# Performance work log

Measured on AMD Instinct MI355X. Metric: run time of the kernel, lower is better.

## Reference

```python
import jax, jax.numpy as jnp
import numpy as np

VOCAB, D_MODEL, N_STATE, H_HEADS, LAYERS = 64, 512, 32, 16, 4
EXPAND = 2
D_INNER = EXPAND * D_MODEL          # 1024
P_HEAD = D_INNER // H_HEADS         # 64
CONV_DIM = D_INNER + 2 * N_STATE    # x, B, C share the depthwise conv
K_CONV = 4
D_IN_PROJ = 2 * D_INNER + 2 * N_STATE + H_HEADS  # z, x, B, C, dt
BATCH, SEQ = 4, 1024
EPS = 1e-5


def rmsnorm(x, w):
    return x * jax.lax.rsqrt(jnp.mean(x * x, axis=-1, keepdims=True) + EPS) * w


def silu(x):
    return x * jax.nn.sigmoid(x)


def causal_depthwise_conv(x, w, b):
    # x: [B,L,C], w: [C,K], b: [C]; causal (left) padding, depthwise groups
    xt = jnp.transpose(x, (0, 2, 1))  # [B,C,L]
    out = jax.lax.conv_general_dilated(xt, w[:, None, :], (1,), [(K_CONV - 1, 0)], feature_group_count=w.shape[0])
    return jnp.transpose(out, (0, 2, 1)) + b


def ssd(xh, dt, A, Bm, Cm, Dp):
    # Mamba2 SSD recurrence. xh [B,L,H,P], dt [B,L,H], A [H], Bm/Cm [B,L,N], Dp [H]
    dA = jnp.exp(dt * A)              # decay per (batch, step, head)
    dtx = dt[..., None] * xh          # [B,L,H,P]

    def step(h, inp):
        dA_t, dtx_t, B_t, C_t = inp
        # h: [B,H,P,N]
        h = dA_t[:, :, None, None] * h + dtx_t[..., None] * B_t[:, None, None, :]
        y = jnp.einsum('bhpn,bn->bhp', h, C_t)
        return h, y

    h0 = jnp.zeros((xh.shape[0], H_HEADS, P_HEAD, N_STATE), xh.dtype)
    _, ys = jax.lax.scan(step, h0, (jnp.moveaxis(dA, 1, 0), jnp.moveaxis(dtx, 1, 0), jnp.moveaxis(Bm, 1, 0), jnp.moveaxis(Cm, 1, 0)))
    return jnp.moveaxis(ys, 0, 1) + xh * Dp[None, None, :, None]


def mamba_block(x, norm_w, W_in, b_in, conv_w, conv_b, dt_bias, A_log, Dp, gnorm_w, W_out, b_out):
    res = x
    u = rmsnorm(x, norm_w)
    zxbcdt = u @ W_in + b_in                                # [B,L,D_IN_PROJ]
    z = zxbcdt[..., :D_INNER]
    xBC = zxbcdt[..., D_INNER:D_INNER + CONV_DIM]
    dt = zxbcdt[..., D_INNER + CONV_DIM:]                   # [B,L,H]
    xBC = silu(causal_depthwise_conv(xBC, conv_w, conv_b))
    xc = xBC[..., :D_INNER]
    Bm = xBC[..., D_INNER:D_INNER + N_STATE]
    Cm = xBC[..., D_INNER + N_STATE:]
    dt = jax.nn.softplus(dt + dt_bias)
    xh = xc.reshape(xc.shape[0], xc.shape[1], H_HEADS, P_HEAD)
    y = ssd(xh, dt, -jnp.exp(A_log), Bm, Cm, Dp)
    y = y.reshape(y.shape[0], y.shape[1], D_INNER)
    y = rmsnorm(y * silu(z), gnorm_w)                       # gated RMSNorm
    return res + y @ W_out + b_out


def forward(input_tokens, emb, norm_w, W_in, b_in, conv_w, conv_b, dt_bias, A_log, D_param, gnorm_w, W_out, b_out, head_w, head_b):
    h = emb[input_tokens]
    for i in range(LAYERS):
        h = mamba_block(h, norm_w[i], W_in[i], b_in[i], conv_w[i], conv_b[i], dt_bias[i], A_log[i], D_param[i], gnorm_w[i], W_out[i], b_out[i])
    return h @ head_w + head_b


def setup_inputs() -> dict:
    key = jax.random.key(0)
    ks = jax.random.split(key, 8)
    s = 0.02
    return {
        'input_tokens': jax.random.randint(ks[0], (BATCH, SEQ), 0, VOCAB),
        'emb': jax.random.normal(ks[1], (VOCAB, D_MODEL), jnp.float32) * s,
        'norm_w': jnp.ones((LAYERS, D_MODEL), jnp.float32),
        'W_in': jax.random.normal(ks[2], (LAYERS, D_MODEL, D_IN_PROJ), jnp.float32) * s,
        'b_in': jnp.zeros((LAYERS, D_IN_PROJ), jnp.float32),
        'conv_w': jax.random.normal(ks[3], (LAYERS, CONV_DIM, K_CONV), jnp.float32) * 0.1,
        'conv_b': jnp.zeros((LAYERS, CONV_DIM), jnp.float32),
        'dt_bias': jnp.tile(jnp.log(jnp.expm1(jnp.linspace(0.001, 0.1, H_HEADS, dtype=jnp.float32))), (LAYERS, 1)),
        'A_log': jnp.tile(jnp.log(jnp.arange(1, H_HEADS + 1, dtype=jnp.float32)), (LAYERS, 1)),
        'D_param': jnp.ones((LAYERS, H_HEADS), jnp.float32),
        'gnorm_w': jnp.ones((LAYERS, D_INNER), jnp.float32),
        'W_out': jax.random.normal(ks[4], (LAYERS, D_INNER, D_MODEL), jnp.float32) * s,
        'b_out': jnp.zeros((LAYERS, D_MODEL), jnp.float32),
        'head_w': jax.random.normal(ks[5], (D_MODEL, VOCAB), jnp.float32) * s,
        'head_b': jnp.zeros((VOCAB,), jnp.float32),
    }


def reference(input_tokens, emb, norm_w, W_in, b_in, conv_w, conv_b, dt_bias, A_log, D_param, gnorm_w, W_out, b_out, head_w, head_b):
    return forward(input_tokens, emb, norm_w, W_in, b_in, conv_w, conv_b, dt_bias, A_log, D_param, gnorm_w, W_out, b_out, head_w, head_b)
```

## Files before the change

kernel.cpp:

```cpp
#include <hip/hip_runtime.h>
#include <hip/hip_bf16.h>

#define VOCAB     64
#define D_MODEL   512
#define N_STATE   32
#define H_HEADS   16
#define LAYERS    4
#define D_INNER   1024
#define P_HEAD    64
#define CONV_DIM  1088
#define K_CONV    4
#define D_IN_PROJ 2128
#define NPAD_IN   2176
#define NPAD_HEAD 64
#define BATCH     4
#define SEQ       1024
#define NTOK      (BATCH*SEQ)
#define EPS       1e-5f
#define CL        64
#define NC        (SEQ/CL)
#define PSTR      80

typedef __bf16 bf16x8 __attribute__((ext_vector_type(8)));
typedef float  f32x4  __attribute__((ext_vector_type(4)));

__device__ __forceinline__ float sigmoidf_(float x) { return 1.f / (1.f + __expf(-x)); }
__device__ __forceinline__ float softplusf_(float x) { return (x > 20.f) ? x : log1pf(__expf(x)); }

__device__ __forceinline__ void gload_lds16(const void* g, void* l) {
  __builtin_amdgcn_global_load_lds((const __attribute__((address_space(1))) void*)g,
                                   (__attribute__((address_space(3))) void*)l,
                                   16, 0, 0);
}

__device__ __forceinline__ int xcd_lin() {
  return (blockIdx.x & 7) * ((int)gridDim.x >> 3) + ((int)blockIdx.x >> 3);
}

__global__ __launch_bounds__(256) void prep_kernel(
    const float* __restrict__ W_in, const float* __restrict__ W_out,
    const float* __restrict__ head_w,
    const float* __restrict__ norm_w, const float* __restrict__ gnorm_w,
    __bf16* __restrict__ WtIn, __bf16* __restrict__ WtOut, __bf16* __restrict__ WtHead,
    const int* __restrict__ tok, const float* __restrict__ emb,
    float* __restrict__ h, __bf16* __restrict__ hbf) {
  int b = blockIdx.x;
  if (b >= 6432) {
    int eb = b - 6432;
    int wv = threadIdx.x >> 6, lane = threadIdx.x & 63;
    int tokid = eb * 4 + wv;
    const float* er = emb + (size_t)tok[tokid] * D_MODEL;
    f32x4 v0 = *(const f32x4*)(er + lane * 8);
    f32x4 v1 = *(const f32x4*)(er + lane * 8 + 4);
    float* hr = h + (size_t)tokid * D_MODEL;
    *(f32x4*)(hr + lane * 8) = v0;
    *(f32x4*)(hr + lane * 8 + 4) = v1;
    bf16x8 o8;
    #pragma unroll
    for (int k = 0; k < 4; k++) { o8[k] = (__bf16)v0[k]; o8[4 + k] = (__bf16)v1[k]; }
    *(bf16x8*)(hbf + (size_t)tokid * D_MODEL + lane * 8) = o8;
    return;
  }
  const float* W; const float* fold; __bf16* Wt; int K, N, Npad, bx, by;
  if (b < 4352) {
    int z = b / 1088, r = b % 1088;
    bx = r % 68; by = r / 68;
    W = W_in + (size_t)z * D_MODEL * D_IN_PROJ;
    fold = norm_w + (size_t)z * D_MODEL;
    Wt = WtIn + (size_t)z * NPAD_IN * D_MODEL;
    K = D_MODEL; N = D_IN_PROJ; Npad = NPAD_IN;
  } else if (b < 6400) {
    int r = b - 4352; int z = r / 512; r %= 512;
    bx = r % 16; by = r / 16;
    W = W_out + (size_t)z * D_INNER * D_MODEL;
    fold = gnorm_w + (size_t)z * D_INNER;
    Wt = WtOut + (size_t)z * D_MODEL * D_INNER;
    K = D_INNER; N = D_MODEL; Npad = D_MODEL;
  } else {
    int r = b - 6400;
    bx = r % 2; by = r / 2;
    W = head_w; fold = nullptr; Wt = WtHead;
    K = D_MODEL; N = VOCAB; Npad = NPAD_HEAD;
  }
  __shared__ float T[32][33];
  int n0 = bx * 32, k0 = by * 32;
  int tx = threadIdx.x & 31, ty = threadIdx.x >> 5;
  #pragma unroll
  for (int i = 0; i < 4; i++) {
    int n = n0 + tx;
    T[ty + i * 8][tx] = (n < N) ? W[(size_t)(k0 + ty + i * 8) * N + n] : 0.f;
  }
  __syncthreads();
  float fs = fold ? fold[k0 + tx] : 1.f;
  #pragma unroll
  for (int i = 0; i < 4; i++)
    Wt[(size_t)(n0 + ty + i * 8) * K + k0 + tx] = (__bf16)(T[tx][ty + i * 8] * fs);
}

#define TK 64
__global__ __launch_bounds__(256) void gemm64_kernel(
    const __bf16* __restrict__ A, const __bf16* __restrict__ Bt,
    const float* __restrict__ bias, const float* __restrict__ res,
    float* __restrict__ C, __bf16* __restrict__ Cbf,
    float inv_norm_dim, int nbx, int K, int N, int ldc) {
  __shared__ __bf16 As[2][64 * TK];
  __shared__ __bf16 Bs[2][64 * TK];
  int tid = threadIdx.x;
  int lane = tid & 63, wave = tid >> 6;
  int wm = wave >> 1, wn = wave & 1;
  int q = lane >> 4, l16 = lane & 15;
  int lin = xcd_lin();
  int bx = lin % nbx, by = lin / nbx;
  size_t row0 = (size_t)by * 64;
  int col0 = bx * 64;
  const __bf16* Ab = A + row0 * K;
  const __bf16* Bb = Bt + (size_t)col0 * K;

  auto stage = [&](int buf, int kk) {
    #pragma unroll
    for (int r = 0; r < 2; r++) {
      int lin2 = r * 256 + tid;
      size_t goff = (size_t)(lin2 >> 3) * K + kk + (lin2 & 7) * 8;
      gload_lds16(Ab + goff, &As[buf][lin2 * 8]);
      gload_lds16(Bb + goff, &Bs[buf][lin2 * 8]);
    }
  };

  f32x4 acc[2][2];
  #pragma unroll
  for (int i = 0; i < 2; i++)
    #pragma unroll
    for (int j = 0; j < 2; j++) acc[i][j] = (f32x4){0.f, 0.f, 0.f, 0.f};
  float ssqa[2] = {0.f, 0.f};

  stage(0, 0);
  int cur = 0;
  for (int k0 = 0; k0 < K; k0 += TK) {
    if (k0 + TK < K) {
      stage(cur ^ 1, k0 + TK);
      asm volatile("s_waitcnt vmcnt(4)" ::: "memory");
    } else {
      asm volatile("s_waitcnt vmcnt(0)" ::: "memory");
    }
    __builtin_amdgcn_s_barrier();
    #pragma unroll
    for (int ks = 0; ks < 2; ks++) {
      bf16x8 af[2], bfv[2];
      #pragma unroll
      for (int i = 0; i < 2; i++) {
        af[i] = *(const bf16x8*)(&As[cur][(wm * 32 + i * 16 + l16) * TK + ks * 32 + q * 8]);
        #pragma unroll
        for (int k = 0; k < 8; k++) { float v = (float)af[i][k]; ssqa[i] += v * v; }
      }
      #pragma unroll
      for (int j = 0; j < 2; j++)
        bfv[j] = *(const bf16x8*)(&Bs[cur][(wn * 32 + j * 16 + l16) * TK + ks * 32 + q * 8]);
      #pragma unroll
      for (int i = 0; i < 2; i++)
        #pragma unroll
        for (int j = 0; j < 2; j++)
          acc[i][j] = __builtin_amdgcn_mfma_f32_16x16x32_bf16(af[i], bfv[j], acc[i][j], 0, 0, 0);
    }
    __builtin_amdgcn_s_barrier();
    cur ^= 1;
  }

  #pragma unroll
  for (int i = 0; i < 2; i++) {
    ssqa[i] += __shfl_xor(ssqa[i], 16);
    ssqa[i] += __shfl_xor(ssqa[i], 32);
  }
  #pragma unroll
  for (int i = 0; i < 2; i++) {
    #pragma unroll
    for (int rr = 0; rr < 4; rr++) {
      size_t mrow = row0 + wm * 32 + i * 16 + q * 4 + rr;
      float sq = __shfl(ssqa[i], q * 4 + rr);
      float sc = (inv_norm_dim > 0.f) ? rsqrtf(sq * inv_norm_dim + EPS) : 1.f;
      #pragma unroll
      for (int j = 0; j < 2; j++) {
        int col = col0 + wn * 32 + j * 16 + l16;
        if (col < N) {
          size_t off = mrow * (size_t)ldc + col;
          float v = acc[i][j][rr] * sc + (bias ? bias[col] : 0.f);
          if (res) v += res[off];
          if (C)   C[off] = v;
          if (Cbf) Cbf[off] = (__bf16)v;
        }
      }
    }
  }
}

__global__ __launch_bounds__(256) void gemm_in_kernel(
    const __bf16* __restrict__ A, const __bf16* __restrict__ Bt,
    const float* __restrict__ bias, __bf16* __restrict__ Cbf,
    int nbx, int K, int N, int ldc) {
  __shared__ __bf16 As[64 * TK];
  __shared__ __bf16 Bs[2][128 * TK];
  int tid = threadIdx.x;
  int lane = tid & 63, wave = tid >> 6;
  int wm = wave >> 1, wn = wave & 1;
  int q = lane >> 4, l16 = lane & 15;
  int lin = xcd_lin();
  int bx = lin % nbx, by = lin / nbx;
  size_t row0 = (size_t)by * 64;
  int col0 = bx * 128;
  const __bf16* Ab = A + row0 * K;
  const __bf16* Bb = Bt + (size_t)col0 * K;

  auto stageA = [&](int kk) {
    #pragma unroll
    for (int r = 0; r < 2; r++) {
      int lin2 = r * 256 + tid;
      gload_lds16(Ab + (size_t)(lin2 >> 3) * K + kk + (lin2 & 7) * 8, As + lin2 * 8);
    }
  };
  auto stageB = [&](int buf, int kk) {
    #pragma unroll
    for (int r = 0; r < 4; r++) {
      int lin2 = r * 256 + tid;
      gload_lds16(Bb + (size_t)(lin2 >> 3) * K + kk + (lin2 & 7) * 8, &Bs[buf][lin2 * 8]);
    }
  };

  f32x4 acc[2][4];
  #pragma unroll
  for (int i = 0; i < 2; i++)
    #pragma unroll
    for (int j = 0; j < 4; j++) acc[i][j] = (f32x4){0.f, 0.f, 0.f, 0.f};
  float ssqa[2] = {0.f, 0.f};

  stageA(0);
  stageB(0, 0);
  int cur = 0;
  for (int k0 = 0; k0 < K; k0 += TK) {
    if (k0 + TK < K) {
      stageB(cur ^ 1, k0 + TK);
      asm volatile("s_waitcnt vmcnt(4)" ::: "memory");
    } else {
      asm volatile("s_waitcnt vmcnt(0)" ::: "memory");
    }
    __builtin_amdgcn_s_barrier();
    #pragma unroll
    for (int ks = 0; ks < 2; ks++) {
      bf16x8 af[2], bfv[4];
      #pragma unroll
      for (int i = 0; i < 2; i++) {
        af[i] = *(const bf16x8*)(&As[(wm * 32 + i * 16 + l16) * TK + ks * 32 + q * 8]);
        #pragma unroll
        for (int k = 0; k < 8; k++) { float v = (float)af[i][k]; ssqa[i] += v * v; }
      }
      #pragma unroll
      for (int j = 0; j < 4; j++)
        bfv[j] = *(const bf16x8*)(&Bs[cur][(wn * 64 + j * 16 + l16) * TK + ks * 32 + q * 8]);
      #pragma unroll
      for (int i = 0; i < 2; i++)
        #pragma unroll
        for (int j = 0; j < 4; j++)
          acc[i][j] = __builtin_amdgcn_mfma_f32_16x16x32_bf16(af[i], bfv[j], acc[i][j], 0, 0, 0);
    }
    __builtin_amdgcn_s_barrier();
    if (k0 + TK < K) stageA(k0 + TK);
    cur ^= 1;
  }

  #pragma unroll
  for (int i = 0; i < 2; i++) {
    ssqa[i] += __shfl_xor(ssqa[i], 16);
    ssqa[i] += __shfl_xor(ssqa[i], 32);
  }
  __bf16* Cs = (__bf16*)Bs;
  const int CST = 136;
  float bvj[4];
  #pragma unroll
  for (int j = 0; j < 4; j++) {
    int colj = col0 + wn * 64 + j * 16 + l16;
    bvj[j] = (colj < N) ? bias[colj] : 0.f;
  }
  #pragma unroll
  for (int i = 0; i < 2; i++) {
    #pragma unroll
    for (int rr = 0; rr < 4; rr++) {
      int rloc = wm * 32 + i * 16 + q * 4 + rr;
      float sq = __shfl(ssqa[i], q * 4 + rr);
      float sc = rsqrtf(sq * (1.f / D_MODEL) + EPS);
      #pragma unroll
      for (int j = 0; j < 4; j++)
        Cs[rloc * CST + wn * 64 + j * 16 + l16] = (__bf16)(acc[i][j][rr] * sc + bvj[j]);
    }
  }
  __syncthreads();
  #pragma unroll
  for (int s = 0; s < 2; s++) {
    int idx = s * 256 + tid;
    int row = idx >> 3, c0 = (idx & 7) * 16;
    if (col0 + c0 < N) {
      bf16x8 v0 = *(const bf16x8*)(&Cs[row * CST + c0]);
      bf16x8 v1 = *(const bf16x8*)(&Cs[row * CST + c0 + 8]);
      __bf16* dst = Cbf + (row0 + row) * (size_t)ldc + col0 + c0;
      *(bf16x8*)dst = v0;
      *(bf16x8*)(dst + 8) = v1;
    }
  }
}

__device__ __forceinline__ void wave0_dt_cumsum(
    const __bf16* __restrict__ zxbf, const float* __restrict__ dt_bias,
    int b, int h, int t0, int tid, float* ldt, float* lcs, float* __restrict__ dtcsg) {
  if (tid < 64) {
    float dv = (float)zxbf[((size_t)(b * SEQ + t0 + tid)) * D_IN_PROJ + 2 * D_INNER + 2 * N_STATE + h]
               + dt_bias[h];
    float dtv = softplusf_(dv);
    float cs = dtv;
    #pragma unroll
    for (int off = 1; off < 64; off <<= 1) {
      float o = __shfl_up(cs, off);
      if (tid >= off) cs += o;
    }
    ldt[tid] = dtv;
    lcs[tid] = cs;
    dtcsg[tid] = dtv;
    dtcsg[64 + tid] = cs;
  }
}

__global__ __launch_bounds__(256) void ssd_local_kernel(
    const __bf16* __restrict__ zxbf, const float* __restrict__ conv_w,
    const float* __restrict__ conv_b, const float* __restrict__ dt_bias,
    const float* __restrict__ A_log,
    float* __restrict__ Slocal, float* __restrict__ dAprod,
    __bf16* __restrict__ convx, __bf16* __restrict__ convbc, float* __restrict__ dtcs) {
  int blk = xcd_lin();
  int c = blk % NC;
  int h = (blk / NC) % H_HEADS;
  int b = blk / (NC * H_HEADS);
  int tid = threadIdx.x;
  int lane = tid & 63, wave = tid >> 6;
  int q = lane >> 4, l16 = lane & 15;
  int t0 = c * CL;
  float A = -__expf(A_log[h]);
  __shared__ __bf16 rawbuf[2 * 68 * 64];
  __shared__ __bf16 lxT[64][PSTR];
  __shared__ __bf16 lBTw[32][PSTR];
  __shared__ float ldt[64], lcs[64];
  __bf16* rawx = rawbuf;
  __bf16* rawBC = rawbuf + 68 * 64;
  for (int i = tid; i < 68 * 8; i += 256) {
    int r = i >> 3, c0 = (i & 7) * 8;
    int gr = t0 - 3 + r;
    bf16x8 vx, vbc;
    #pragma unroll
    for (int k = 0; k < 8; k++) { vx[k] = (__bf16)0.f; vbc[k] = (__bf16)0.f; }
    if (gr >= 0) {
      const __bf16* rowp = zxbf + ((size_t)(b * SEQ + gr)) * D_IN_PROJ;
      vx  = *(const bf16x8*)(rowp + D_INNER + h * 64 + c0);
      vbc = *(const bf16x8*)(rowp + 2 * D_INNER + c0);
    }
    *(bf16x8*)(rawx + r * 64 + c0)  = vx;
    *(bf16x8*)(rawBC + r * 64 + c0) = vbc;
  }
  wave0_dt_cumsum(zxbf, dt_bias, b, h, t0, tid, ldt, lcs, dtcs + (size_t)blk * 128);
  __syncthreads();
  float cs63 = lcs[63];
  __bf16* xg  = convx  + (size_t)blk * (64 * PSTR);
  __bf16* bcg = convbc + (size_t)blk * 4096;
  {
    int p = tid & 63;
    const float* w = conv_w + (h * 64 + p) * K_CONV;
    float w0 = w[0], w1 = w[1], w2 = w[2], w3 = w[3];
    float cb = conv_b[h * 64 + p];
    for (int i = tid; i < CL * 64; i += 256) {
      int t = i >> 6;
      float a = cb + w0 * (float)rawx[t * 64 + p] + w1 * (float)rawx[(t + 1) * 64 + p]
                   + w2 * (float)rawx[(t + 2) * 64 + p] + w3 * (float)rawx[(t + 3) * 64 + p];
      lxT[p][t] = (__bf16)(a * sigmoidf_(a));
    }
  }
  {
    int col = tid & 63;
    const float* w = conv_w + (D_INNER + col) * K_CONV;
    float w0 = w[0], w1 = w[1], w2 = w[2], w3 = w[3];
    float cb = conv_b[D_INNER + col];
    for (int i = tid; i < CL * 64; i += 256) {
      int t = i >> 6;
      float a = cb + w0 * (float)rawBC[t * 64 + col] + w1 * (float)rawBC[(t + 1) * 64 + col]
                   + w2 * (float)rawBC[(t + 2) * 64 + col] + w3 * (float)rawBC[(t + 3) * 64 + col];
      float v = a * sigmoidf_(a);
      if (col < 32) {
        bcg[t * 32 + col] = (__bf16)v;
        float wt = ldt[t] * __expf(A * (cs63 - lcs[t]));
        lBTw[col][t] = (__bf16)(v * wt);
      } else {
        bcg[2048 + t * 32 + (col - 32)] = (__bf16)v;
      }
    }
  }
  __syncthreads();
  for (int i = tid; i < (64 * PSTR) / 8; i += 256)
    *(bf16x8*)(xg + i * 8) = *(const bf16x8*)(((const __bf16*)lxT) + i * 8);
  if (c < NC - 1) {
    f32x4 acc0 = (f32x4){0.f,0.f,0.f,0.f}, acc1 = (f32x4){0.f,0.f,0.f,0.f};
    #pragma unroll
    for (int kb = 0; kb < 2; kb++) {
      bf16x8 af = *(const bf16x8*)(&lxT[wave * 16 + l16][kb * 32 + q * 8]);
      bf16x8 b0 = *(const bf16x8*)(&lBTw[l16][kb * 32 + q * 8]);
      bf16x8 b1 = *(const bf16x8*)(&lBTw[l16 + 16][kb * 32 + q * 8]);
      acc0 = __builtin_amdgcn_mfma_f32_16x16x32_bf16(af, b0, acc0, 0, 0, 0);
      acc1 = __builtin_amdgcn_mfma_f32_16x16x32_bf16(af, b1, acc1, 0, 0, 0);
    }
    float* sT = (float*)rawbuf;
    #pragma unroll
    for (int rr = 0; rr < 4; rr++) {
      int p = wave * 16 + q * 4 + rr;
      sT[p * 36 + l16]      = acc0[rr];
      sT[p * 36 + l16 + 16] = acc1[rr];
    }
    int row = tid >> 2, c0 = (tid & 3) * 8;
    f32x4 a = *(const f32x4*)(sT + row * 36 + c0);
    f32x4 b2 = *(const f32x4*)(sT + row * 36 + c0 + 4);
    float* dstp = Slocal + (size_t)blk * 2048 + row * 32 + c0;
    *(f32x4*)dstp = a;
    *(f32x4*)(dstp + 4) = b2;
  }
  if (tid == 0) dAprod[blk] = __expf(A * cs63);
}

__global__ __launch_bounds__(256) void ssd_out_kernel(
    const __bf16* __restrict__ zxbf, const float* __restrict__ A_log,
    const float* __restrict__ Dp,
    const float* __restrict__ Slocal, const float* __restrict__ dAprod,
    const __bf16* __restrict__ convx, const __bf16* __restrict__ convbc,
    const float* __restrict__ dtcs, __bf16* __restrict__ gout) {
  int blk = xcd_lin();
  int c = blk % NC;
  int h = (blk / NC) % H_HEADS;
  int b = blk / (NC * H_HEADS);
  int tid = threadIdx.x;
  int lane = tid & 63, wave = tid >> 6;
  int q = lane >> 4, l16 = lane & 15;
  int t0 = c * CL;
  float A = -__expf(A_log[h]);
  float D = Dp[h];
  __shared__ __bf16 lxT[64][PSTR];
  __shared__ __bf16 pPbuf[64 * PSTR];
  __shared__ __bf16 lBC[2 * 64 * 32];
  __shared__ __bf16 lS[64][32];
  __shared__ float ldt[64], lcs[64];
  const __bf16* xg  = convx  + (size_t)blk * (64 * PSTR);
  const __bf16* bcg = convbc + (size_t)blk * 4096;
  __bf16* lB = lBC;
  __bf16* lC = lBC + 2048;
  for (int i = tid; i < (64 * PSTR) / 8; i += 256)
    gload_lds16(xg + i * 8, ((__bf16*)lxT) + i * 8);
  for (int i = tid; i < 512; i += 256)
    gload_lds16(bcg + i * 8, lBC + i * 8);
  if (tid < 64) {
    const float* dg = dtcs + (size_t)blk * 128;
    ldt[tid] = dg[tid];
    lcs[tid] = dg[64 + tid];
  }
  {
    int p = tid >> 2, n0 = (tid & 3) * 8;
    const float* sl = Slocal + (size_t)(blk - c) * 2048 + p * 32 + n0;
    const float* dab = dAprod + (blk - c);
    float st[8] = {};
    for (int j = 0; j < c; j++) {
      f32x4 a = *(const f32x4*)(sl + (size_t)j * 2048);
      f32x4 bq = *(const f32x4*)(sl + (size_t)j * 2048 + 4);
      float prj = dab[j];
      #pragma unroll
      for (int k = 0; k < 4; k++) { st[k] = prj * st[k] + a[k]; st[4 + k] = prj * st[4 + k] + bq[k]; }
    }
    #pragma unroll
    for (int k = 0; k < 8; k++) lS[p][n0 + k] = (__bf16)st[k];
  }
  __syncthreads();
  bf16x8 afC = *(const bf16x8*)(lC + (wave * 16 + l16) * 32 + q * 8);
  f32x4 accG[4], accI[4], accY[4];
  #pragma unroll
  for (int j = 0; j < 4; j++) {
    accG[j] = (f32x4){0.f,0.f,0.f,0.f};
    accI[j] = (f32x4){0.f,0.f,0.f,0.f};
    accY[j] = (f32x4){0.f,0.f,0.f,0.f};
  }
  #pragma unroll
  for (int j = 0; j < 4; j++) {
    bf16x8 bf = *(const bf16x8*)(lB + (l16 + 16 * j) * 32 + q * 8);
    accG[j] = __builtin_amdgcn_mfma_f32_16x16x32_bf16(afC, bf, accG[j], 0, 0, 0);
  }
  #pragma unroll
  for (int j = 0; j < 4; j++) {
    bf16x8 bf = *(const bf16x8*)(&lS[l16 + 16 * j][q * 8]);
    accI[j] = __builtin_amdgcn_mfma_f32_16x16x32_bf16(afC, bf, accI[j], 0, 0, 0);
  }
  __bf16* pP = pPbuf + wave * 16 * PSTR;
  #pragma unroll
  for (int j = 0; j < 4; j++) {
    int s = l16 + 16 * j;
    float css = lcs[s], dts = ldt[s];
    #pragma unroll
    for (int rr = 0; rr < 4; rr++) {
      int tl = q * 4 + rr;
      int t = wave * 16 + tl;
      float val = accG[j][rr] * __expf(A * (lcs[t] - css)) * dts;
      if (s == t) val += D;
      if (s > t) val = 0.f;
      pP[tl * PSTR + s] = (__bf16)val;
    }
  }
  #pragma unroll
  for (int kb = 0; kb < 2; kb++) {
    bf16x8 afP = *(const bf16x8*)(pP + l16 * PSTR + kb * 32 + q * 8);
    #pragma unroll
    for (int j = 0; j < 4; j++) {
      bf16x8 bf = *(const bf16x8*)(&lxT[l16 + 16 * j][kb * 32 + q * 8]);
      accY[j] = __builtin_amdgcn_mfma_f32_16x16x32_bf16(afP, bf, accY[j], 0, 0, 0);
    }
  }
  __syncthreads();
  __bf16* yT = pPbuf;
  #pragma unroll
  for (int rr = 0; rr < 4; rr++) {
    int t = wave * 16 + q * 4 + rr;
    float cumt = __expf(A * lcs[t]);
    #pragma unroll
    for (int j = 0; j < 4; j++) {
      int p = l16 + 16 * j;
      yT[t * 72 + p] = (__bf16)(accY[j][rr] + cumt * accI[j][rr]);
    }
  }
  {
    int row = tid >> 2, col0 = (tid & 3) * 16;
    bf16x8 y0 = *(const bf16x8*)(yT + row * 72 + col0);
    bf16x8 y1 = *(const bf16x8*)(yT + row * 72 + col0 + 8);
    const __bf16* zrow = zxbf + ((size_t)(b * SEQ + t0 + row)) * D_IN_PROJ + h * 64 + col0;
    bf16x8 z0 = *(const bf16x8*)zrow;
    bf16x8 z1 = *(const bf16x8*)(zrow + 8);
    bf16x8 g0, g1;
    #pragma unroll
    for (int k = 0; k < 8; k++) {
      float zz = (float)z0[k];
      g0[k] = (__bf16)((float)y0[k] * zz * sigmoidf_(zz));
    }
    #pragma unroll
    for (int k = 0; k < 8; k++) {
      float zz = (float)z1[k];
      g1[k] = (__bf16)((float)y1[k] * zz * sigmoidf_(zz));
    }
    __bf16* grow = gout + ((size_t)(b * SEQ + t0 + row)) * D_INNER + h * 64 + col0;
    *(bf16x8*)grow = g0;
    *(bf16x8*)(grow + 8) = g1;
  }
}

extern "C" void kernel_launch(void* const* d_in, const int* in_sizes, int n_in,
                              void* d_out, int out_size, void* d_ws, size_t ws_size,
                              hipStream_t stream) {
  const int*   tok     = (const int*)  d_in[0];
  const float* emb     = (const float*)d_in[1];
  const float* norm_w  = (const float*)d_in[2];
  const float* W_in    = (const float*)d_in[3];
  const float* b_in    = (const float*)d_in[4];
  const float* conv_w  = (const float*)d_in[5];
  const float* conv_b  = (const float*)d_in[6];
  const float* dt_bias = (const float*)d_in[7];
  const float* A_log   = (const float*)d_in[8];
  const float* D_par   = (const float*)d_in[9];
  const float* gnorm_w = (const float*)d_in[10];
  const float* W_out   = (const float*)d_in[11];
  const float* b_out   = (const float*)d_in[12];
  const float* head_w  = (const float*)d_in[13];
  const float* head_b  = (const float*)d_in[14];
  float* out = (float*)d_out;

  char* p = (char*)d_ws;
  auto alloc = [&](size_t bytes) { void* r = (void*)p; p += (bytes + 255) & ~(size_t)255; return r; };
  float*  h      = (float*) alloc((size_t)NTOK * D_MODEL * 4);
  float*  slocal = (float*) alloc((size_t)BATCH * H_HEADS * NC * P_HEAD * N_STATE * 4);
  float*  daprod = (float*) alloc((size_t)BATCH * H_HEADS * NC * 4);
  float*  dtcs   = (float*) alloc((size_t)1024 * 128 * 4);
  __bf16* convx  = (__bf16*)alloc((size_t)1024 * 64 * PSTR * 2);
  __bf16* convbc = (__bf16*)alloc((size_t)1024 * 4096 * 2);
  __bf16* zxbf   = (__bf16*)alloc((size_t)NTOK * D_IN_PROJ * 2);
  __bf16* gbf    = (__bf16*)alloc((size_t)NTOK * D_INNER * 2);
  __bf16* hbf    = (__bf16*)alloc((size_t)NTOK * D_MODEL * 2);
  __bf16* WtIn   = (__bf16*)alloc((size_t)LAYERS * NPAD_IN * D_MODEL * 2);
  __bf16* WtOut  = (__bf16*)alloc((size_t)LAYERS * D_MODEL * D_INNER * 2);
  __bf16* WtHead = (__bf16*)alloc((size_t)NPAD_HEAD * D_MODEL * 2);

  prep_kernel<<<6432 + NTOK / 4, 256, 0, stream>>>(
      W_in, W_out, head_w, norm_w, gnorm_w, WtIn, WtOut, WtHead,
      tok, emb, h, hbf);

  for (int l = 0; l < LAYERS; l++) {
    gemm_in_kernel<<<1088, 256, 0, stream>>>(
        hbf, WtIn + (size_t)l * NPAD_IN * D_MODEL, b_in + (size_t)l * D_IN_PROJ,
        zxbf, NPAD_IN / 128, D_MODEL, D_IN_PROJ, D_IN_PROJ);

    ssd_local_kernel<<<BATCH * H_HEADS * NC, 256, 0, stream>>>(
        zxbf, conv_w + (size_t)l * CONV_DIM * K_CONV, conv_b + (size_t)l * CONV_DIM,
        dt_bias + (size_t)l * H_HEADS, A_log + (size_t)l * H_HEADS, slocal, daprod,
        convx, convbc, dtcs);
    ssd_out_kernel<<<BATCH * H_HEADS * NC, 256, 0, stream>>>(
        zxbf, A_log + (size_t)l * H_HEADS, D_par + (size_t)l * H_HEADS,
        slocal, daprod, convx, convbc, dtcs, gbf);

    gemm64_kernel<<<512, 256, 0, stream>>>(
        gbf, WtOut + (size_t)l * D_MODEL * D_INNER, b_out + (size_t)l * D_MODEL, h,
        h, hbf, 1.f / D_INNER, D_MODEL / 64, D_INNER, D_MODEL, D_MODEL);
  }

  gemm64_kernel<<<64, 256, 0, stream>>>(
      hbf, WtHead, head_b, nullptr, out, nullptr, 0.f, 1, D_MODEL, VOCAB, VOCAB);
}
```

Measured before the change: 445.1 us.

## Narrow gemm64 tile to 64x32 and triple-buffer the LDS staging

The out-projection and head GEMM now use 64x32 output tiles instead of 64x64, which doubles the grid to 1024 and 128 blocks so more CUs have work. The LDS pipeline moves from double to triple buffering with two stages kept in flight, and the vmcnt waits are adjusted to match. Each block now reloads its A tile for half as many outputs, and the fused RMS sum of squares is recomputed per block, so A-side traffic and redundant work go up in exchange for parallelism and latency hiding.

```diff
diff --git a/kernel.cpp b/kernel.cpp
--- a/kernel.cpp
+++ b/kernel.cpp
@@ -103,8 +103,8 @@
     const float* __restrict__ bias, const float* __restrict__ res,
     float* __restrict__ C, __bf16* __restrict__ Cbf,
     float inv_norm_dim, int nbx, int K, int N, int ldc) {
-  __shared__ __bf16 As[2][64 * TK];
-  __shared__ __bf16 Bs[2][64 * TK];
+  __shared__ __bf16 As[3][64 * TK];
+  __shared__ __bf16 Bs[3][32 * TK];
   int tid = threadIdx.x;
   int lane = tid & 63, wave = tid >> 6;
   int wm = wave >> 1, wn = wave & 1;
@@ -112,7 +112,7 @@
   int lin = xcd_lin();
   int bx = lin % nbx, by = lin / nbx;
   size_t row0 = (size_t)by * 64;
-  int col0 = bx * 64;
+  int col0 = bx * 32;
   const __bf16* Ab = A + row0 * K;
   const __bf16* Bb = Bt + (size_t)col0 * K;
 
@@ -120,49 +120,49 @@
     #pragma unroll
     for (int r = 0; r < 2; r++) {
       int lin2 = r * 256 + tid;
-      size_t goff = (size_t)(lin2 >> 3) * K + kk + (lin2 & 7) * 8;
-      gload_lds16(Ab + goff, &As[buf][lin2 * 8]);
-      gload_lds16(Bb + goff, &Bs[buf][lin2 * 8]);
+      gload_lds16(Ab + (size_t)(lin2 >> 3) * K + kk + (lin2 & 7) * 8, &As[buf][lin2 * 8]);
+    }
+    {
+      int lin2 = tid;
+      gload_lds16(Bb + (size_t)(lin2 >> 3) * K + kk + (lin2 & 7) * 8, &Bs[buf][lin2 * 8]);
     }
   };
 
-  f32x4 acc[2][2];
-  #pragma unroll
-  for (int i = 0; i < 2; i++)
-    #pragma unroll
-    for (int j = 0; j < 2; j++) acc[i][j] = (f32x4){0.f, 0.f, 0.f, 0.f};
+  f32x4 acc[2];
+  acc[0] = (f32x4){0.f, 0.f, 0.f, 0.f};
+  acc[1] = (f32x4){0.f, 0.f, 0.f, 0.f};
   float ssqa[2] = {0.f, 0.f};
 
+  int niter = K / TK;
   stage(0, 0);
-  int cur = 0;
-  for (int k0 = 0; k0 < K; k0 += TK) {
-    if (k0 + TK < K) {
-      stage(cur ^ 1, k0 + TK);
-      asm volatile("s_waitcnt vmcnt(4)" ::: "memory");
+  if (niter > 1) stage(1, TK);
+  int bi = 0;
+  for (int i = 0; i < niter; i++) {
+    if (i + 2 < niter) {
+      stage((bi + 2) % 3, (i + 2) * TK);
+      asm volatile("s_waitcnt vmcnt(6)" ::: "memory");
+    } else if (i + 1 < niter) {
+      asm volatile("s_waitcnt vmcnt(3)" ::: "memory");
     } else {
       asm volatile("s_waitcnt vmcnt(0)" ::: "memory");
     }
     __builtin_amdgcn_s_barrier();
     #pragma unroll
     for (int ks = 0; ks < 2; ks++) {
-      bf16x8 af[2], bfv[2];
+      bf16x8 af[2], bfv;
       #pragma unroll
-      for (int i = 0; i < 2; i++) {
-        af[i] = *(const bf16x8*)(&As[cur][(wm * 32 + i * 16 + l16) * TK + ks * 32 + q * 8]);
+      for (int ii = 0; ii < 2; ii++) {
+        af[ii] = *(const bf16x8*)(&As[bi][(wm * 32 + ii * 16 + l16) * TK + ks * 32 + q * 8]);
         #pragma unroll
-        for (int k = 0; k < 8; k++) { float v = (float)af[i][k]; ssqa[i] += v * v; }
+        for (int k = 0; k < 8; k++) { float v = (float)af[ii][k]; ssqa[ii] += v * v; }
       }
+      bfv = *(const bf16x8*)(&Bs[bi][(wn * 16 + l16) * TK + ks * 32 + q * 8]);
       #pragma unroll
-      for (int j = 0; j < 2; j++)
-        bfv[j] = *(const bf16x8*)(&Bs[cur][(wn * 32 + j * 16 + l16) * TK + ks * 32 + q * 8]);
-      #pragma unroll
-      for (int i = 0; i < 2; i++)
-        #pragma unroll
-        for (int j = 0; j < 2; j++)
-          acc[i][j] = __builtin_amdgcn_mfma_f32_16x16x32_bf16(af[i], bfv[j], acc[i][j], 0, 0, 0);
+      for (int ii = 0; ii < 2; ii++)
+        acc[ii] = __builtin_amdgcn_mfma_f32_16x16x32_bf16(af[ii], bfv, acc[ii], 0, 0, 0);
     }
     __builtin_amdgcn_s_barrier();
-    cur ^= 1;
+    bi = (bi + 1) % 3;
   }
 
   #pragma unroll
@@ -177,16 +177,13 @@
       size_t mrow = row0 + wm * 32 + i * 16 + q * 4 + rr;
       float sq = __shfl(ssqa[i], q * 4 + rr);
       float sc = (inv_norm_dim > 0.f) ? rsqrtf(sq * inv_norm_dim + EPS) : 1.f;
-      #pragma unroll
-      for (int j = 0; j < 2; j++) {
-        int col = col0 + wn * 32 + j * 16 + l16;
-        if (col < N) {
-          size_t off = mrow * (size_t)ldc + col;
-          float v = acc[i][j][rr] * sc + (bias ? bias[col] : 0.f);
-          if (res) v += res[off];
-          if (C)   C[off] = v;
-          if (Cbf) Cbf[off] = (__bf16)v;
-        }
+      int col = col0 + wn * 16 + l16;
+      if (col < N) {
+        size_t off = mrow * (size_t)ldc + col;
+        float v = acc[i][rr] * sc + (bias ? bias[col] : 0.f);
+        if (res) v += res[off];
+        if (C)   C[off] = v;
+        if (Cbf) Cbf[off] = (__bf16)v;
       }
     }
   }
@@ -606,11 +603,11 @@
         zxbf, A_log + (size_t)l * H_HEADS, D_par + (size_t)l * H_HEADS,
         slocal, daprod, convx, convbc, dtcs, gbf);
 
-    gemm64_kernel<<<512, 256, 0, stream>>>(
+    gemm64_kernel<<<1024, 256, 0, stream>>>(
         gbf, WtOut + (size_t)l * D_MODEL * D_INNER, b_out + (size_t)l * D_MODEL, h,
-        h, hbf, 1.f / D_INNER, D_MODEL / 64, D_INNER, D_MODEL, D_MODEL);
-  }
-
-  gemm64_kernel<<<64, 256, 0, stream>>>(
-      hbf, WtHead, head_b, nullptr, out, nullptr, 0.f, 1, D_MODEL, VOCAB, VOCAB);
-}
+        h, hbf, 1.f / D_INNER, D_MODEL / 32, D_INNER, D_MODEL, D_MODEL);
+  }
+
+  gemm64_kernel<<<128, 256, 0, stream>>>(
+      hbf, WtHead, head_b, nullptr, out, nullptr, 0.f, NPAD_HEAD / 32, D_MODEL, VOCAB, VOCAB);
+}
```

Result: faster. 431.9 us, median of 2 (-3.0%).
